# Performance work log

Measured on AMD Instinct MI355X. Metric: run time of the kernel, lower is better.

The kernel has to match this reference:

```python
import jax, jax.numpy as jnp
import numpy as np

HEADS = 16
DIM_HEAD = 64
SCALE = DIM_HEAD ** -0.5
NEG = -jnp.finfo(jnp.float32).max


def setup_inputs() -> dict:
    key = jax.random.key(0)
    ks = jax.random.split(key, 5)
    b, n, dim = 2, 2048, 1024
    inner = HEADS * DIM_HEAD
    s = dim ** -0.5  # keep pre-softmax logits well-scaled
    return {
        "x": jax.random.normal(ks[0], (b, n, dim), jnp.float32),
        "mask": jnp.ones((b, n), dtype=bool),
        "Wq": jax.random.normal(ks[1], (dim, inner), jnp.float32) * s,
        "Wk": jax.random.normal(ks[2], (dim, inner), jnp.float32) * s,
        "Wv": jax.random.normal(ks[3], (dim, inner), jnp.float32) * s,
        "Wo": jax.random.normal(ks[4], (inner, dim), jnp.float32) * s,
    }


def reference(x, mask, Wq, Wk, Wv, Wo):
    b, n, _ = x.shape
    # projections, split heads: b n (h d) -> b h n d
    def split(t):
        return t.reshape(b, n, HEADS, DIM_HEAD).transpose(0, 2, 1, 3)
    q = split(x @ Wq)
    k = split(x @ Wk)
    v = split(x @ Wv)
    dots = jnp.einsum("bhid,bhjd->bhij", q, k) * SCALE  # [b,h,n,n]
    # padding mask: b j -> b 1 1 j
    dots = jnp.where(mask[:, None, None, :], dots, NEG)
    # causal mask (strict upper triangle masked)
    causal = jnp.triu(jnp.ones((n, n), dtype=bool), k=1)
    dots = jnp.where(causal, NEG, dots)
    attn = jax.nn.softmax(dots, axis=-1)
    out = jnp.einsum("bhij,bhjd->bhid", attn, v)
    out = out.transpose(0, 2, 1, 3).reshape(b, n, HEADS * DIM_HEAD)
    return out @ Wo
```

## Files before the change

kernel.cpp:

```cpp
#include <hip/hip_runtime.h>
#include <hip/hip_bf16.h>

typedef __bf16 bf16x8 __attribute__((ext_vector_type(8)));
typedef float f32x4 __attribute__((ext_vector_type(4)));
typedef unsigned short u16;
typedef unsigned int u32;

#define MFMA16(A, B, C) __builtin_amdgcn_mfma_f32_16x16x32_bf16((A), (B), (C), 0, 0, 0)

#define BATCH 2
#define SEQ   2048
#define DIM   1024
#define NHEAD 16
#define DHEAD 64
#define MROWS 4096
#define Q_SCALE 0.18033688f

__device__ __forceinline__ u16 f2bf(float f) {
    unsigned int u = __float_as_uint(f);
    u += 0x7fff + ((u >> 16) & 1);
    return (u16)(u >> 16);
}

__device__ __forceinline__ u32 pk2bf(float a, float b) {
    __hip_bfloat162 c = __float22bfloat162_rn(float2{a, b});
    u32 r;
    __builtin_memcpy(&r, &c, 4);
    return r;
}

__device__ __forceinline__ void glds16(const u16* g, u16* l) {
    __builtin_amdgcn_global_load_lds(
        (const __attribute__((address_space(1))) u32*)g,
        (__attribute__((address_space(3))) u32*)l, 16, 0, 0);
}

__global__ __launch_bounds__(256) void prep(const float* __restrict__ x,
                                            const float* __restrict__ wq,
                                            const float* __restrict__ wk,
                                            const float* __restrict__ wv,
                                            const float* __restrict__ wo,
                                            u16* __restrict__ xb,
                                            u16* __restrict__ wt) {
    const int b = blockIdx.x;
    const int t = threadIdx.x;
    if (b < 2048) {
        int i = (b * 256 + t) * 8;
        float4 a = *(const float4*)(x + i);
        float4 c = *(const float4*)(x + i + 4);
        u16 o[8] = {f2bf(a.x), f2bf(a.y), f2bf(a.z), f2bf(a.w),
                    f2bf(c.x), f2bf(c.y), f2bf(c.z), f2bf(c.w)};
        *(uint4*)(xb + i) = *(uint4*)o;
        return;
    }
    __shared__ u16 tile[64][65];
    const int bb = b - 2048;
    const int z = bb >> 8, rem = bb & 255;
    const float* W = (z == 0) ? wq : (z == 1) ? wk : (z == 2) ? wv : wo;
    u16* out = wt + (size_t)z * DIM * DIM;
    int k0 = (rem & 15) * 64;
    int n0 = (rem >> 4) * 64;
    int c = t & 63, r4 = t >> 6;
#pragma unroll
    for (int i = 0; i < 16; i++) {
        int row = i * 4 + r4;
        tile[row][c] = f2bf(W[(size_t)(k0 + row) * DIM + n0 + c]);
    }
    __syncthreads();
#pragma unroll
    for (int i = 0; i < 16; i++) {
        int row = i * 4 + r4;
        out[(size_t)(n0 + row) * DIM + k0 + c] = tile[c][row];
    }
}

__global__ __launch_bounds__(256) void gemm_qkv(const u16* __restrict__ xb,
                                                const u16* __restrict__ wt,
                                                u16* __restrict__ qb,
                                                u16* __restrict__ kb,
                                                u16* __restrict__ vtb) {
    __shared__ __align__(16) u16 As[128 * 32];
    __shared__ __align__(16) u16 Bs[128 * 32];
    const int z = blockIdx.z;
    const u16* W = wt + (size_t)z * DIM * DIM;
    const int m0 = blockIdx.y * 128, n0 = blockIdx.x * 128;
    const int t = threadIdx.x, w = t >> 6, lane = t & 63;
    const int quad = lane >> 4, l16 = lane & 15;
    const int wm = (w >> 1) * 64, wn = (w & 1) * 64;
    const int srow = lane >> 2, skc = (lane & 3) * 8;

    f32x4 acc[4][4] = {};
    for (int k0 = 0; k0 < DIM; k0 += 32) {
        if (k0) __syncthreads();
#pragma unroll
        for (int j = 0; j < 2; j++) {
            int rb = w * 32 + j * 16;
            glds16(&xb[(size_t)(m0 + rb + srow) * DIM + k0 + skc], &As[rb * 32]);
            glds16(&W[(size_t)(n0 + rb + srow) * DIM + k0 + skc], &Bs[rb * 32]);
        }
        __syncthreads();

        bf16x8 af[4], bfr[4];
#pragma unroll
        for (int mt = 0; mt < 4; mt++)
            af[mt] = *(const bf16x8*)&As[(wm + mt * 16 + l16) * 32 + quad * 8];
#pragma unroll
        for (int nt = 0; nt < 4; nt++)
            bfr[nt] = *(const bf16x8*)&Bs[(wn + nt * 16 + l16) * 32 + quad * 8];
#pragma unroll
        for (int mt = 0; mt < 4; mt++)
#pragma unroll
            for (int nt = 0; nt < 4; nt++)
                acc[mt][nt] = MFMA16(af[mt], bfr[nt], acc[mt][nt]);
    }
    const float sc = (z == 0) ? Q_SCALE : 1.0f;
#pragma unroll
    for (int mt = 0; mt < 4; mt++)
#pragma unroll
        for (int nt = 0; nt < 4; nt++)
#pragma unroll
            for (int r = 0; r < 4; r++) {
                int gm = m0 + wm + mt * 16 + quad * 4 + r;
                int gc = n0 + wn + nt * 16 + l16;
                int bi = gm >> 11, si = gm & (SEQ - 1);
                int h = gc >> 6, d = gc & 63;
                u16 v = f2bf(acc[mt][nt][r] * sc);
                if (z == 0)
                    qb[(((size_t)bi * NHEAD + h) * SEQ + si) * DHEAD + d] = v;
                else if (z == 1)
                    kb[(((size_t)bi * NHEAD + h) * SEQ + si) * DHEAD + d] = v;
                else
                    vtb[(((size_t)bi * NHEAD + h) * DHEAD + d) * SEQ + si] = v;
            }
}

#define LPAD 72
#define OSTR 68
__global__ __launch_bounds__(256) void attn(const u16* __restrict__ qg,
                                            const u16* __restrict__ kg,
                                            const u16* __restrict__ vtg,
                                            u16* __restrict__ og) {
    __shared__ __align__(16) u16 Ks[2][64 * LPAD];
    __shared__ __align__(16) u16 Vs[2][64 * LPAD];
    __shared__ __align__(16) u16 Ps[64 * LPAD];
    __shared__ __align__(16) float Os[64 * OSTR];
    __shared__ float Ls[64];

    const int linear = blockIdx.x;
    const int kidx = linear >> 3;
    const int bh = (linear & 7) * 4 + (kidx >> 4);
    const int px = kidx & 15;
    const int t = threadIdx.x, w = t >> 6, lane = t & 63;
    const int quad = lane >> 4, l16 = lane & 15;
    const int wq32 = (w >> 1) * 32, kh = w & 1, kh32 = kh * 32;
    const int srow = t >> 2, sc16 = (t & 3) * 16;
    const size_t qkbase = (size_t)bh * SEQ;
    const size_t vbase = (size_t)bh * DHEAD;
    const int bi = bh >> 4, hh = bh & 15;

    uint4 pk0, pk1, pv0, pv1;
    auto prefetch = [&](int j0) {
        const u16* kp = &kg[(qkbase + j0 + srow) * DHEAD + sc16];
        pk0 = *(const uint4*)kp;
        pk1 = *(const uint4*)(kp + 8);
        const u16* vp = &vtg[(vbase + srow) * SEQ + j0 + sc16];
        pv0 = *(const uint4*)vp;
        pv1 = *(const uint4*)(vp + 8);
    };

    for (int half = 0; half < 2; half++) {
        const int qt = half ? (31 - px) : px;
        const int q0 = qt * 64;
        const int last = qt;
        const int rowmin = q0 + wq32;

        bf16x8 bq[2][2];
#pragma unroll
        for (int ct = 0; ct < 2; ct++) {
            const u16* qp = qg + (qkbase + q0 + wq32 + ct * 16 + l16) * DHEAD;
            bq[ct][0] = *(const bf16x8*)(qp + quad * 8);
            bq[ct][1] = *(const bf16x8*)(qp + 32 + quad * 8);
        }

        f32x4 accO[4][2] = {};
        float l_part[2] = {0.f, 0.f};

        prefetch(0);
        __syncthreads();

        for (int jt = 0; jt <= last; jt++) {
            const int buf = jt & 1;
            u16* ksb = &Ks[buf][0];
            u16* vsb = &Vs[buf][0];
            *(uint4*)&ksb[srow * LPAD + sc16] = pk0;
            *(uint4*)&ksb[srow * LPAD + sc16 + 8] = pk1;
            *(uint4*)&vsb[srow * LPAD + sc16] = pv0;
            *(uint4*)&vsb[srow * LPAD + sc16 + 8] = pv1;
            __syncthreads();
            if (jt < last) prefetch((jt + 1) * 64);

            const int j0 = jt * 64;
            if (j0 + kh32 > rowmin + 31) continue;
            const bool need_mask = (j0 + kh32 + 31 > rowmin);

            bf16x8 ak[2][2];
#pragma unroll
            for (int nt = 0; nt < 2; nt++) {
                const u16* kr = &ksb[(kh32 + nt * 16 + l16) * LPAD];
                ak[nt][0] = *(const bf16x8*)(kr + quad * 8);
                ak[nt][1] = *(const bf16x8*)(kr + 32 + quad * 8);
            }
            f32x4 s[2][2];
#pragma unroll
            for (int nt = 0; nt < 2; nt++)
#pragma unroll
                for (int ct = 0; ct < 2; ct++) {
                    f32x4 a = {};
                    a = MFMA16(ak[nt][0], bq[ct][0], a);
                    a = MFMA16(ak[nt][1], bq[ct][1], a);
                    s[nt][ct] = a;
                }

            if (need_mask) {
#pragma unroll
                for (int ct = 0; ct < 2; ct++) {
                    int qv = q0 + wq32 + ct * 16 + l16;
#pragma unroll
                    for (int nt = 0; nt < 2; nt++) {
                        int kb = j0 + kh32 + nt * 16 + quad * 4;
                        float p[4];
#pragma unroll
                        for (int r = 0; r < 4; r++)
                            p[r] = (kb + r > qv) ? 0.f
                                 : __builtin_amdgcn_exp2f(s[nt][ct][r]);
                        l_part[ct] += (p[0] + p[1]) + (p[2] + p[3]);
                        uint2 pkd = {pk2bf(p[0], p[1]), pk2bf(p[2], p[3])};
                        *(uint2*)&Ps[(wq32 + ct * 16 + l16) * LPAD + kh32 +
                                     nt * 16 + quad * 4] = pkd;
                    }
                }
            } else {
#pragma unroll
                for (int ct = 0; ct < 2; ct++)
#pragma unroll
                    for (int nt = 0; nt < 2; nt++) {
                        float p[4];
#pragma unroll
                        for (int r = 0; r < 4; r++)
                            p[r] = __builtin_amdgcn_exp2f(s[nt][ct][r]);
                        l_part[ct] += (p[0] + p[1]) + (p[2] + p[3]);
                        uint2 pkd = {pk2bf(p[0], p[1]), pk2bf(p[2], p[3])};
                        *(uint2*)&Ps[(wq32 + ct * 16 + l16) * LPAD + kh32 +
                                     nt * 16 + quad * 4] = pkd;
                    }
            }

            bf16x8 bp[2];
#pragma unroll
            for (int ct = 0; ct < 2; ct++)
                bp[ct] = *(const bf16x8*)&Ps[(wq32 + ct * 16 + l16) * LPAD +
                                             kh32 + quad * 8];
#pragma unroll
            for (int mt = 0; mt < 4; mt++) {
                bf16x8 av = *(const bf16x8*)&vsb[(mt * 16 + l16) * LPAD +
                                                 kh32 + quad * 8];
#pragma unroll
                for (int ct = 0; ct < 2; ct++)
                    accO[mt][ct] = MFMA16(av, bp[ct], accO[mt][ct]);
            }
        }

        float l2[2];
#pragma unroll
        for (int ct = 0; ct < 2; ct++) {
            float l = l_part[ct];
            l += __shfl_xor(l, 16);
            l += __shfl_xor(l, 32);
            l2[ct] = l;
        }
        if (kh == 1) {
            if (quad == 0) {
                Ls[wq32 + l16] = l2[0];
                Ls[wq32 + 16 + l16] = l2[1];
            }
#pragma unroll
            for (int mt = 0; mt < 4; mt++)
#pragma unroll
                for (int ct = 0; ct < 2; ct++)
                    *(float4*)&Os[(wq32 + ct * 16 + l16) * OSTR + mt * 16 +
                                  quad * 4] =
                        float4{accO[mt][ct][0], accO[mt][ct][1],
                               accO[mt][ct][2], accO[mt][ct][3]};
        }
        __syncthreads();
        if (kh == 0) {
#pragma unroll
            for (int ct = 0; ct < 2; ct++) {
                int q = q0 + wq32 + ct * 16 + l16;
                float rl = 1.0f / (l2[ct] + Ls[wq32 + ct * 16 + l16]);
                size_t obase = ((size_t)bi * SEQ + q) * DIM + hh * DHEAD;
#pragma unroll
                for (int mt = 0; mt < 4; mt++) {
                    float4 o = *(float4*)&Os[(wq32 + ct * 16 + l16) * OSTR +
                                             mt * 16 + quad * 4];
                    float v0 = (accO[mt][ct][0] + o.x) * rl;
                    float v1 = (accO[mt][ct][1] + o.y) * rl;
                    float v2 = (accO[mt][ct][2] + o.z) * rl;
                    float v3 = (accO[mt][ct][3] + o.w) * rl;
                    uint2 pkd = {pk2bf(v0, v1), pk2bf(v2, v3)};
                    *(uint2*)&og[obase + mt * 16 + quad * 4] = pkd;
                }
            }
        }
    }
}

__global__ __launch_bounds__(256) void gemm_out(const u16* __restrict__ ob,
                                                const u16* __restrict__ wot,
                                                float* __restrict__ out) {
    __shared__ __align__(16) u16 As[64 * 32];
    __shared__ __align__(16) u16 Bs[128 * 32];
    const int m0 = blockIdx.y * 64, n0 = blockIdx.x * 128;
    const int t = threadIdx.x, w = t >> 6, lane = t & 63;
    const int quad = lane >> 4, l16 = lane & 15;
    const int wm = (w >> 1) * 32, wn = (w & 1) * 64;
    const int srow = lane >> 2, skc = (lane & 3) * 8;

    f32x4 acc[2][4] = {};
    for (int k0 = 0; k0 < DIM; k0 += 32) {
        if (k0) __syncthreads();
        glds16(&ob[(size_t)(m0 + w * 16 + srow) * DIM + k0 + skc], &As[w * 16 * 32]);
#pragma unroll
        for (int j = 0; j < 2; j++) {
            int rb = w * 32 + j * 16;
            glds16(&wot[(size_t)(n0 + rb + srow) * DIM + k0 + skc], &Bs[rb * 32]);
        }
        __syncthreads();

        bf16x8 af[2], bfr[4];
#pragma unroll
        for (int mt = 0; mt < 2; mt++)
            af[mt] = *(const bf16x8*)&As[(wm + mt * 16 + l16) * 32 + quad * 8];
#pragma unroll
        for (int nt = 0; nt < 4; nt++)
            bfr[nt] = *(const bf16x8*)&Bs[(wn + nt * 16 + l16) * 32 + quad * 8];
#pragma unroll
        for (int mt = 0; mt < 2; mt++)
#pragma unroll
            for (int nt = 0; nt < 4; nt++)
                acc[mt][nt] = MFMA16(af[mt], bfr[nt], acc[mt][nt]);
    }
#pragma unroll
    for (int mt = 0; mt < 2; mt++)
#pragma unroll
        for (int nt = 0; nt < 4; nt++)
#pragma unroll
            for (int r = 0; r < 4; r++) {
                int gm = m0 + wm + mt * 16 + quad * 4 + r;
                int gc = n0 + wn + nt * 16 + l16;
                out[(size_t)gm * DIM + gc] = acc[mt][nt][r];
            }
}

extern "C" void kernel_launch(void* const* d_in, const int* in_sizes, int n_in,
                              void* d_out, int out_size, void* d_ws, size_t ws_size,
                              hipStream_t stream) {
    const float* x  = (const float*)d_in[0];
    const float* wq = (const float*)d_in[2];
    const float* wk = (const float*)d_in[3];
    const float* wv = (const float*)d_in[4];
    const float* wo = (const float*)d_in[5];
    float* out = (float*)d_out;

    char* ws = (char*)d_ws;
    u16* xb  = (u16*)(ws);
    u16* wt  = (u16*)(ws + (8ull  << 20));
    u16* qb  = (u16*)(ws + (16ull << 20));
    u16* kb  = (u16*)(ws + (24ull << 20));
    u16* vtb = (u16*)(ws + (32ull << 20));
    u16* obf = (u16*)(ws + (40ull << 20));

    prep<<<3072, 256, 0, stream>>>(x, wq, wk, wv, wo, xb, wt);
    gemm_qkv<<<dim3(DIM / 128, MROWS / 128, 3), 256, 0, stream>>>(xb, wt, qb, kb, vtb);
    attn<<<512, 256, 0, stream>>>(qb, kb, vtb, obf);
    gemm_out<<<dim3(DIM / 128, MROWS / 64), 256, 0, stream>>>(
        obf, wt + 3ull * DIM * DIM, out);
}
```

Measured before the change: 177.4 us.

## Rewrite QKV GEMM as 256x256 tile, 8-wave, double-buffered pipelined kernel

```diff
diff --git a/kernel.cpp b/kernel.cpp
--- a/kernel.cpp
+++ b/kernel.cpp
@@ -74,54 +74,165 @@
     }
 }
 
-__global__ __launch_bounds__(256) void gemm_qkv(const u16* __restrict__ xb,
-                                                const u16* __restrict__ wt,
-                                                u16* __restrict__ qb,
-                                                u16* __restrict__ kb,
-                                                u16* __restrict__ vtb) {
-    __shared__ __align__(16) u16 As[128 * 32];
-    __shared__ __align__(16) u16 Bs[128 * 32];
-    const int z = blockIdx.z;
-    const u16* W = wt + (size_t)z * DIM * DIM;
-    const int m0 = blockIdx.y * 128, n0 = blockIdx.x * 128;
+__global__ __launch_bounds__(512, 2) void gemm_qkv(const u16* __restrict__ xb,
+                                                   const u16* __restrict__ wt,
+                                                   u16* __restrict__ qb,
+                                                   u16* __restrict__ kb,
+                                                   u16* __restrict__ vtb) {
+    __shared__ __align__(16) u16 As[2 * 256 * 64];
+    __shared__ __align__(16) u16 Bs[2 * 256 * 64];
+
+    const int bid = blockIdx.x;
+    const int wg = (bid & 7) * 24 + (bid >> 3);
+    const int mb = wg / 12, nb = wg % 12;
+    const int m0 = mb * 256;
+    const int n0g = nb * 256;
+
     const int t = threadIdx.x, w = t >> 6, lane = t & 63;
     const int quad = lane >> 4, l16 = lane & 15;
-    const int wm = (w >> 1) * 64, wn = (w & 1) * 64;
-    const int srow = lane >> 2, skc = (lane & 3) * 8;
-
-    f32x4 acc[4][4] = {};
-    for (int k0 = 0; k0 < DIM; k0 += 32) {
-        if (k0) __syncthreads();
-#pragma unroll
-        for (int j = 0; j < 2; j++) {
-            int rb = w * 32 + j * 16;
-            glds16(&xb[(size_t)(m0 + rb + srow) * DIM + k0 + skc], &As[rb * 32]);
-            glds16(&W[(size_t)(n0 + rb + srow) * DIM + k0 + skc], &Bs[rb * 32]);
-        }
-        __syncthreads();
-
-        bf16x8 af[4], bfr[4];
-#pragma unroll
-        for (int mt = 0; mt < 4; mt++)
-            af[mt] = *(const bf16x8*)&As[(wm + mt * 16 + l16) * 32 + quad * 8];
+    const int wr = w >> 2, wc = w & 3;
+
+    const int srow0 = w * 8 + (lane >> 3);
+    const int srow1 = (8 + w) * 8 + (lane >> 3);
+    const int scol = ((lane & 7) ^ (lane >> 3)) * 8;
+    const u16* Apan = xb + (size_t)m0 * DIM;
+    const u16* Bpan = wt + (size_t)n0g * DIM;
+
+    auto stage = [&](const u16* pan, int rbase, int kc, u16* dhalf) {
+        glds16(pan + (size_t)(rbase + srow0) * DIM + kc + scol, dhalf + w * 512);
+        glds16(pan + (size_t)(rbase + srow1) * DIM + kc + scol,
+               dhalf + (8 + w) * 512);
+    };
+
+    const int fo0 = ((0 * 4 + quad) ^ (l16 & 7)) * 8;
+    const int fo1 = ((4 + quad) ^ (l16 & 7)) * 8;
+    u16* const A0h = As + wr * 8192;
+    u16* const A1h = As + 16384 + wr * 8192;
+    u16* const B0h = Bs + (wc >> 1) * 8192;
+    u16* const B1h = Bs + 16384 + (wc >> 1) * 8192;
+    const int bRow0 = (wc & 1) * 64;
+
+#define RD_A(MH, AH)                                                          \
+    do {                                                                      \
+        _Pragma("unroll") for (int i = 0; i < 4; i++) {                       \
+            const u16* p = (AH) + (((MH) * 4 + i) * 16 + l16) * 64;           \
+            a[i][0] = *(const bf16x8*)(p + fo0);                              \
+            a[i][1] = *(const bf16x8*)(p + fo1);                              \
+        }                                                                     \
+    } while (0)
+
+#define RD_B(NH, BH, BSET)                                                    \
+    do {                                                                      \
+        _Pragma("unroll") for (int j = 0; j < 2; j++) {                       \
+            const u16* p = (BH) + (bRow0 + ((NH) * 2 + j) * 16 + l16) * 64;   \
+            BSET[j][0] = *(const bf16x8*)(p + fo0);                           \
+            BSET[j][1] = *(const bf16x8*)(p + fo1);                           \
+        }                                                                     \
+    } while (0)
+
+#define MM(MH, NH, BSET)                                                      \
+    do {                                                                      \
+        __builtin_amdgcn_s_setprio(1);                                        \
+        _Pragma("unroll") for (int i = 0; i < 4; i++)                         \
+            _Pragma("unroll") for (int j = 0; j < 2; j++) {                   \
+            acc[(MH) * 4 + i][(NH) * 2 + j] =                                 \
+                MFMA16(a[i][0], BSET[j][0], acc[(MH) * 4 + i][(NH) * 2 + j]); \
+            acc[(MH) * 4 + i][(NH) * 2 + j] =                                 \
+                MFMA16(a[i][1], BSET[j][1], acc[(MH) * 4 + i][(NH) * 2 + j]); \
+        }                                                                     \
+        __builtin_amdgcn_s_setprio(0);                                        \
+    } while (0)
+
+#define SBAR()                                                                \
+    do {                                                                      \
+        __builtin_amdgcn_sched_barrier(0);                                    \
+        __builtin_amdgcn_s_barrier();                                         \
+        __builtin_amdgcn_sched_barrier(0);                                    \
+    } while (0)
+
+#define VMW(N)                                                                \
+    do {                                                                      \
+        __builtin_amdgcn_sched_barrier(0);                                    \
+        asm volatile("s_waitcnt vmcnt(" #N ")" ::: "memory");                 \
+        __builtin_amdgcn_sched_barrier(0);                                    \
+    } while (0)
+
+    f32x4 acc[8][4] = {};
+    bf16x8 a[4][2], bA[2][2], bB[2][2];
+
+    stage(Bpan, 0, 0, Bs);
+    stage(Apan, 0, 0, As);
+    stage(Apan, 128, 0, As + 8192);
+    stage(Bpan, 128, 0, Bs + 8192);
+    stage(Bpan, 0, 64, Bs + 16384);
+    stage(Apan, 0, 64, As + 16384);
+    VMW(4);
+    SBAR();
+
+#pragma unroll 1
+    for (int i = 0; i < 8; i++) {
+        const int kc1 = (2 * i + 1) * 64;
+        const int kc2 = (2 * i + 2) * 64;
+        const int kc3 = (2 * i + 3) * 64;
+        const bool g2 = (2 * i + 2) < 16;
+        const bool g3 = (2 * i + 3) < 16;
+
+        RD_A(0, A0h);
+        RD_B(0, B0h, bA);
+        stage(Bpan, 128, kc1, Bs + 16384 + 8192);
+        SBAR();
+        MM(0, 0, bA);
+        SBAR();
+        RD_B(1, B0h, bB);
+        stage(Apan, 128, kc1, As + 16384 + 8192);
+        SBAR();
+        MM(0, 1, bB);
+        SBAR();
+        RD_A(1, A0h);
+        if (g2) stage(Bpan, 0, kc2, Bs);
+        SBAR();
+        MM(1, 1, bB);
+        SBAR();
+        if (g2) stage(Apan, 0, kc2, As);
+        SBAR();
+        MM(1, 0, bA);
+        VMW(4);
+        SBAR();
+
+        RD_A(0, A1h);
+        RD_B(0, B1h, bA);
+        if (g2) stage(Apan, 128, kc2, As + 8192);
+        SBAR();
+        MM(0, 0, bA);
+        SBAR();
+        RD_B(1, B1h, bB);
+        if (g2) stage(Bpan, 128, kc2, Bs + 8192);
+        SBAR();
+        MM(0, 1, bB);
+        SBAR();
+        RD_A(1, A1h);
+        if (g3) stage(Bpan, 0, kc3, Bs + 16384);
+        SBAR();
+        MM(1, 1, bB);
+        SBAR();
+        if (g3) stage(Apan, 0, kc3, As + 16384);
+        SBAR();
+        MM(1, 0, bA);
+        VMW(4);
+        SBAR();
+    }
+
+    const int z = n0g >> 10;
+    const int nin = n0g & 1023;
+    const float sc = (z == 0) ? Q_SCALE : 1.0f;
+#pragma unroll
+    for (int mt = 0; mt < 8; mt++)
 #pragma unroll
         for (int nt = 0; nt < 4; nt++)
-            bfr[nt] = *(const bf16x8*)&Bs[(wn + nt * 16 + l16) * 32 + quad * 8];
-#pragma unroll
-        for (int mt = 0; mt < 4; mt++)
-#pragma unroll
-            for (int nt = 0; nt < 4; nt++)
-                acc[mt][nt] = MFMA16(af[mt], bfr[nt], acc[mt][nt]);
-    }
-    const float sc = (z == 0) ? Q_SCALE : 1.0f;
-#pragma unroll
-    for (int mt = 0; mt < 4; mt++)
-#pragma unroll
-        for (int nt = 0; nt < 4; nt++)
 #pragma unroll
             for (int r = 0; r < 4; r++) {
-                int gm = m0 + wm + mt * 16 + quad * 4 + r;
-                int gc = n0 + wn + nt * 16 + l16;
+                int gm = m0 + wr * 128 + mt * 16 + quad * 4 + r;
+                int gc = nin + wc * 64 + nt * 16 + l16;
                 int bi = gm >> 11, si = gm & (SEQ - 1);
                 int h = gc >> 6, d = gc & 63;
                 u16 v = f2bf(acc[mt][nt][r] * sc);
@@ -132,6 +243,11 @@
                 else
                     vtb[(((size_t)bi * NHEAD + h) * DHEAD + d) * SEQ + si] = v;
             }
+#undef RD_A
+#undef RD_B
+#undef MM
+#undef SBAR
+#undef VMW
 }
 
 #define LPAD 72
@@ -215,10 +331,10 @@
             for (int nt = 0; nt < 2; nt++)
 #pragma unroll
                 for (int ct = 0; ct < 2; ct++) {
-                    f32x4 a = {};
-                    a = MFMA16(ak[nt][0], bq[ct][0], a);
-                    a = MFMA16(ak[nt][1], bq[ct][1], a);
-                    s[nt][ct] = a;
+                    f32x4 aa = {};
+                    aa = MFMA16(ak[nt][0], bq[ct][0], aa);
+                    aa = MFMA16(ak[nt][1], bq[ct][1], aa);
+                    s[nt][ct] = aa;
                 }
 
             if (need_mask) {
@@ -381,7 +497,7 @@
     u16* obf = (u16*)(ws + (40ull << 20));
 
     prep<<<3072, 256, 0, stream>>>(x, wq, wk, wv, wo, xb, wt);
-    gemm_qkv<<<dim3(DIM / 128, MROWS / 128, 3), 256, 0, stream>>>(xb, wt, qb, kb, vtb);
+    gemm_qkv<<<192, 512, 0, stream>>>(xb, wt, qb, kb, vtb);
     attn<<<512, 256, 0, stream>>>(qb, kb, vtb, obf);
     gemm_out<<<dim3(DIM / 128, MROWS / 64), 256, 0, stream>>>(
         obf, wt + 3ull * DIM * DIM, out);
```

Measured after the change: 200.9 us. 1.13x slower.

## Deepen GEMM K-tiles to 64 with XOR-swizzled LDS and staged V-transpose stores

Applied to the files above, without the earlier changes.

```diff
diff --git a/kernel.cpp b/kernel.cpp
--- a/kernel.cpp
+++ b/kernel.cpp
@@ -79,59 +79,94 @@
                                                 u16* __restrict__ qb,
                                                 u16* __restrict__ kb,
                                                 u16* __restrict__ vtb) {
-    __shared__ __align__(16) u16 As[128 * 32];
-    __shared__ __align__(16) u16 Bs[128 * 32];
+    __shared__ __align__(16) u16 SMEM[17408];
+    u16* const As = SMEM;
+    u16* const Bs = SMEM + 8192;
+
     const int z = blockIdx.z;
-    const u16* W = wt + (size_t)z * DIM * DIM;
+    const u16* Apan = xb;
+    const u16* Bpan = wt + (size_t)z * DIM * DIM;
     const int m0 = blockIdx.y * 128, n0 = blockIdx.x * 128;
     const int t = threadIdx.x, w = t >> 6, lane = t & 63;
     const int quad = lane >> 4, l16 = lane & 15;
     const int wm = (w >> 1) * 64, wn = (w & 1) * 64;
-    const int srow = lane >> 2, skc = (lane & 3) * 8;
+    const int srow = lane >> 3;
+    const int scol = ((lane & 7) ^ srow) * 8;
+    const int fo0 = ((quad) ^ (l16 & 7)) * 8;
+    const int fo1 = ((4 + quad) ^ (l16 & 7)) * 8;
 
     f32x4 acc[4][4] = {};
-    for (int k0 = 0; k0 < DIM; k0 += 32) {
+    for (int k0 = 0; k0 < DIM; k0 += 64) {
         if (k0) __syncthreads();
 #pragma unroll
-        for (int j = 0; j < 2; j++) {
-            int rb = w * 32 + j * 16;
-            glds16(&xb[(size_t)(m0 + rb + srow) * DIM + k0 + skc], &As[rb * 32]);
-            glds16(&W[(size_t)(n0 + rb + srow) * DIM + k0 + skc], &Bs[rb * 32]);
-        }
-        __syncthreads();
-
-        bf16x8 af[4], bfr[4];
+        for (int j = 0; j < 4; j++) {
+            int rb = w * 32 + j * 8;
+            glds16(Apan + (size_t)(m0 + rb + srow) * DIM + k0 + scol, &As[rb * 64]);
+            glds16(Bpan + (size_t)(n0 + rb + srow) * DIM + k0 + scol, &Bs[rb * 64]);
+        }
+        __syncthreads();
+
+        bf16x8 af[4][2], bfr[4][2];
+#pragma unroll
+        for (int mt = 0; mt < 4; mt++) {
+            const u16* p = &As[(wm + mt * 16 + l16) * 64];
+            af[mt][0] = *(const bf16x8*)(p + fo0);
+            af[mt][1] = *(const bf16x8*)(p + fo1);
+        }
+#pragma unroll
+        for (int nt = 0; nt < 4; nt++) {
+            const u16* p = &Bs[(wn + nt * 16 + l16) * 64];
+            bfr[nt][0] = *(const bf16x8*)(p + fo0);
+            bfr[nt][1] = *(const bf16x8*)(p + fo1);
+        }
 #pragma unroll
         for (int mt = 0; mt < 4; mt++)
-            af[mt] = *(const bf16x8*)&As[(wm + mt * 16 + l16) * 32 + quad * 8];
-#pragma unroll
-        for (int nt = 0; nt < 4; nt++)
-            bfr[nt] = *(const bf16x8*)&Bs[(wn + nt * 16 + l16) * 32 + quad * 8];
+#pragma unroll
+            for (int nt = 0; nt < 4; nt++) {
+                acc[mt][nt] = MFMA16(af[mt][0], bfr[nt][0], acc[mt][nt]);
+                acc[mt][nt] = MFMA16(af[mt][1], bfr[nt][1], acc[mt][nt]);
+            }
+    }
+
+    const int bi = m0 >> 11;
+    if (z < 2) {
+        const float sc = (z == 0) ? Q_SCALE : 1.0f;
+        u16* dst = (z == 0) ? qb : kb;
 #pragma unroll
         for (int mt = 0; mt < 4; mt++)
 #pragma unroll
             for (int nt = 0; nt < 4; nt++)
-                acc[mt][nt] = MFMA16(af[mt], bfr[nt], acc[mt][nt]);
-    }
-    const float sc = (z == 0) ? Q_SCALE : 1.0f;
-#pragma unroll
-    for (int mt = 0; mt < 4; mt++)
-#pragma unroll
-        for (int nt = 0; nt < 4; nt++)
-#pragma unroll
-            for (int r = 0; r < 4; r++) {
-                int gm = m0 + wm + mt * 16 + quad * 4 + r;
-                int gc = n0 + wn + nt * 16 + l16;
-                int bi = gm >> 11, si = gm & (SEQ - 1);
-                int h = gc >> 6, d = gc & 63;
-                u16 v = f2bf(acc[mt][nt][r] * sc);
-                if (z == 0)
-                    qb[(((size_t)bi * NHEAD + h) * SEQ + si) * DHEAD + d] = v;
-                else if (z == 1)
-                    kb[(((size_t)bi * NHEAD + h) * SEQ + si) * DHEAD + d] = v;
-                else
-                    vtb[(((size_t)bi * NHEAD + h) * DHEAD + d) * SEQ + si] = v;
-            }
+#pragma unroll
+                for (int r = 0; r < 4; r++) {
+                    int gm = m0 + wm + mt * 16 + quad * 4 + r;
+                    int gc = n0 + wn + nt * 16 + l16;
+                    int si = gm & (SEQ - 1);
+                    int h = gc >> 6, d = gc & 63;
+                    dst[(((size_t)bi * NHEAD + h) * SEQ + si) * DHEAD + d] =
+                        f2bf(acc[mt][nt][r] * sc);
+                }
+    } else {
+        __syncthreads();
+        u16* T = SMEM;
+#pragma unroll
+        for (int mt = 0; mt < 4; mt++)
+#pragma unroll
+            for (int nt = 0; nt < 4; nt++)
+#pragma unroll
+                for (int r = 0; r < 4; r++)
+                    T[(wn + nt * 16 + l16) * 136 + wm + mt * 16 + quad * 4 + r] =
+                        f2bf(acc[mt][nt][r]);
+        __syncthreads();
+        const int row = t >> 1;
+        const int half = (t & 1) * 64;
+        const int gc = n0 + row;
+        const int h = gc >> 6, d = gc & 63;
+        const size_t gb = (((size_t)bi * NHEAD + h) * DHEAD + d) * SEQ +
+                          (m0 & (SEQ - 1)) + half;
+#pragma unroll
+        for (int i = 0; i < 8; i++)
+            *(uint4*)&vtb[gb + i * 8] = *(const uint4*)&T[row * 136 + half + i * 8];
+    }
 }
 
 #define LPAD 72
@@ -215,10 +250,10 @@
             for (int nt = 0; nt < 2; nt++)
 #pragma unroll
                 for (int ct = 0; ct < 2; ct++) {
-                    f32x4 a = {};
-                    a = MFMA16(ak[nt][0], bq[ct][0], a);
-                    a = MFMA16(ak[nt][1], bq[ct][1], a);
-                    s[nt][ct] = a;
+                    f32x4 aa = {};
+                    aa = MFMA16(ak[nt][0], bq[ct][0], aa);
+                    aa = MFMA16(ak[nt][1], bq[ct][1], aa);
+                    s[nt][ct] = aa;
                 }
 
             if (need_mask) {
@@ -318,37 +353,52 @@
 __global__ __launch_bounds__(256) void gemm_out(const u16* __restrict__ ob,
                                                 const u16* __restrict__ wot,
                                                 float* __restrict__ out) {
-    __shared__ __align__(16) u16 As[64 * 32];
-    __shared__ __align__(16) u16 Bs[128 * 32];
+    __shared__ __align__(16) u16 As[64 * 64];
+    __shared__ __align__(16) u16 Bs[128 * 64];
     const int m0 = blockIdx.y * 64, n0 = blockIdx.x * 128;
     const int t = threadIdx.x, w = t >> 6, lane = t & 63;
     const int quad = lane >> 4, l16 = lane & 15;
     const int wm = (w >> 1) * 32, wn = (w & 1) * 64;
-    const int srow = lane >> 2, skc = (lane & 3) * 8;
+    const int srow = lane >> 3;
+    const int scol = ((lane & 7) ^ srow) * 8;
+    const int fo0 = ((quad) ^ (l16 & 7)) * 8;
+    const int fo1 = ((4 + quad) ^ (l16 & 7)) * 8;
 
     f32x4 acc[2][4] = {};
-    for (int k0 = 0; k0 < DIM; k0 += 32) {
+    for (int k0 = 0; k0 < DIM; k0 += 64) {
         if (k0) __syncthreads();
-        glds16(&ob[(size_t)(m0 + w * 16 + srow) * DIM + k0 + skc], &As[w * 16 * 32]);
 #pragma unroll
         for (int j = 0; j < 2; j++) {
-            int rb = w * 32 + j * 16;
-            glds16(&wot[(size_t)(n0 + rb + srow) * DIM + k0 + skc], &Bs[rb * 32]);
-        }
-        __syncthreads();
-
-        bf16x8 af[2], bfr[4];
+            int rb = w * 16 + j * 8;
+            glds16(&ob[(size_t)(m0 + rb + srow) * DIM + k0 + scol], &As[rb * 64]);
+        }
+#pragma unroll
+        for (int j = 0; j < 4; j++) {
+            int rb = w * 32 + j * 8;
+            glds16(&wot[(size_t)(n0 + rb + srow) * DIM + k0 + scol], &Bs[rb * 64]);
+        }
+        __syncthreads();
+
+        bf16x8 af[2][2], bfr[4][2];
+#pragma unroll
+        for (int mt = 0; mt < 2; mt++) {
+            const u16* p = &As[(wm + mt * 16 + l16) * 64];
+            af[mt][0] = *(const bf16x8*)(p + fo0);
+            af[mt][1] = *(const bf16x8*)(p + fo1);
+        }
+#pragma unroll
+        for (int nt = 0; nt < 4; nt++) {
+            const u16* p = &Bs[(wn + nt * 16 + l16) * 64];
+            bfr[nt][0] = *(const bf16x8*)(p + fo0);
+            bfr[nt][1] = *(const bf16x8*)(p + fo1);
+        }
 #pragma unroll
         for (int mt = 0; mt < 2; mt++)
-            af[mt] = *(const bf16x8*)&As[(wm + mt * 16 + l16) * 32 + quad * 8];
-#pragma unroll
-        for (int nt = 0; nt < 4; nt++)
-            bfr[nt] = *(const bf16x8*)&Bs[(wn + nt * 16 + l16) * 32 + quad * 8];
-#pragma unroll
-        for (int mt = 0; mt < 2; mt++)
-#pragma unroll
-            for (int nt = 0; nt < 4; nt++)
-                acc[mt][nt] = MFMA16(af[mt], bfr[nt], acc[mt][nt]);
+#pragma unroll
+            for (int nt = 0; nt < 4; nt++) {
+                acc[mt][nt] = MFMA16(af[mt][0], bfr[nt][0], acc[mt][nt]);
+                acc[mt][nt] = MFMA16(af[mt][1], bfr[nt][1], acc[mt][nt]);
+            }
     }
 #pragma unroll
     for (int mt = 0; mt < 2; mt++)
```

Measured after the change: 166.5 us. 1.07x faster.
